# Performance work log

Measured on AMD Instinct MI355X. Metric: run time of the kernel, lower is better.

Reference implementation:

```python
import jax, jax.numpy as jnp
import numpy as np

S = 10  # samples per node


def setup_inputs() -> dict:
    key = jax.random.key(0)
    k1, k2, k3, k4, k5, k6 = jax.random.split(key, 6)
    N, D, V, E, NNZ = 8192, 256, 32768, 100000, 262144
    z = jax.random.normal(k1, (N, D), dtype=jnp.float32)
    W = jax.random.normal(k2, (V, D), dtype=jnp.float32) * 0.02
    rand_u = jax.random.uniform(k3, (N, S), dtype=jnp.float32)
    edges = jax.random.randint(k4, (2, E), 0, N, dtype=jnp.int64)
    ptr = jnp.sort(jax.random.randint(k5, (N + 1,), 0, NNZ, dtype=jnp.int64))
    col = jax.random.randint(k6, (NNZ,), 0, N, dtype=jnp.int64)
    return {"z": z, "W": W, "rand_u": rand_u, "edges": edges, "ptr": ptr, "col": col}


def reference(z, W, rand_u, edges, ptr, col):
    N = z.shape[0]
    nnz = col.shape[0]
    deg = ptr[1:] - ptr[:-1]                                   # [N]
    # vectorized per-node uniform neighbor sampling (with replacement)
    samp = (rand_u * deg[:, None].astype(rand_u.dtype)).astype(jnp.int64)  # [N, S]
    gidx = jnp.clip(ptr[:-1, None] + samp, 0, nnz - 1)          # [N, S]
    self_idx = jnp.arange(N, dtype=col.dtype)[:, None]
    n_u = jnp.where(deg[:, None] > 0, col[gidx], self_idx)      # [N, S]
    # gather-sum aggregation, averaged with self
    u_aggr = (z[n_u].sum(axis=1) + z) / (S + 1)                 # [N, D]
    # predictor: Linear(no bias) + Softmax(dim=1)
    logits = jnp.einsum('nd,vd->nv', u_aggr, W)                 # [N, V]
    probs = jax.nn.softmax(logits, axis=1)
    h_u = probs[edges[0]]                                       # [E, V]
    # nn.CrossEntropyLoss applied to softmax outputs (faithful to original)
    tgt = edges[1]
    log_p = jax.nn.log_softmax(h_u, axis=1)
    loss = -log_p[jnp.arange(tgt.shape[0]), tgt].mean()
    return loss
```

## Files before the change

### kernel.cpp

```cpp
#include <hip/hip_runtime.h>
#include <hip/hip_bf16.h>
#include <stdint.h>


#define NODES 8192
#define DIM   256
#define VOCAB 32768
#define SAMP  10

typedef float  f32x4  __attribute__((ext_vector_type(4)));
typedef short  bf16x8 __attribute__((ext_vector_type(8)));
typedef unsigned short u16x4 __attribute__((ext_vector_type(4)));

static __device__ __forceinline__ unsigned short f2bf(float x) {
    __hip_bfloat16 b = __float2bfloat16(x);
    return *reinterpret_cast<unsigned short*>(&b);
}
static __device__ __forceinline__ float bf2f(unsigned short x) {
    union { unsigned int u; float f; } v; v.u = ((unsigned int)x) << 16; return v.f;
}

__global__ void k_aggregate(const float* __restrict__ z, const float* __restrict__ ru,
                            const int* __restrict__ ptr, const int* __restrict__ col,
                            unsigned short* __restrict__ ub, int nnz) {
    int wid = threadIdx.x >> 6, lane = threadIdx.x & 63;
    int node = blockIdx.x * 4 + wid;
    if (node >= NODES) return;
    int p0 = ptr[node], p1 = ptr[node + 1];
    int deg = p1 - p0;
    float fdeg = (float)deg;
    f32x4 acc = {0.f, 0.f, 0.f, 0.f};
    #pragma unroll
    for (int s = 0; s < SAMP; ++s) {
        float r = ru[node * SAMP + s];
        int samp = (int)(r * fdeg);
        int gidx = p0 + samp;
        gidx = gidx < 0 ? 0 : (gidx > nnz - 1 ? nnz - 1 : gidx);
        int nb = (deg > 0) ? col[gidx] : node;
        acc += ((const f32x4*)(z + (size_t)nb * DIM))[lane];
    }
    acc += ((const f32x4*)(z + (size_t)node * DIM))[lane];
    acc = acc / 11.0f;
    u16x4 h;
    h.x = f2bf(acc.x); h.y = f2bf(acc.y); h.z = f2bf(acc.z); h.w = f2bf(acc.w);
    ((u16x4*)(ub + (size_t)node * DIM))[lane] = h;
}

__global__ void k_convert_w(const float* __restrict__ W, unsigned short* __restrict__ Wb, int n4) {
    int i = blockIdx.x * blockDim.x + threadIdx.x;
    if (i >= n4) return;
    f32x4 v = ((const f32x4*)W)[i];
    u16x4 h;
    h.x = f2bf(v.x); h.y = f2bf(v.y); h.z = f2bf(v.z); h.w = f2bf(v.w);
    ((u16x4*)Wb)[i] = h;
}

#define BM 128
#define BN 256
#define NSTEP 64

static __device__ __forceinline__ void gload_lds16(const void* g, void* l) {
    __builtin_amdgcn_global_load_lds(
        (const __attribute__((address_space(1))) unsigned int*)g,
        (__attribute__((address_space(3))) unsigned int*)l, 16, 0, 0);
}

__global__ __launch_bounds__(512, 2) void k_gemm_stats(
        const unsigned short* __restrict__ A,
        const unsigned short* __restrict__ B,
        float* __restrict__ part_s) {
    __shared__ __align__(16) unsigned short Bs[3][BN * 64];
    __shared__ float sred[BM][4];

    const int bid = blockIdx.x;
    const int slab = bid & 7;
    const int ntile = bid >> 3;
    const int rm = ntile * BM;
    const int cbase = slab * 4096;
    const int t = threadIdx.x;
    const int lane = t & 63;
    const int wid = t >> 6;
    const int wr = wid >> 2, wc = wid & 3;
    const int g = lane >> 4, r16 = lane & 15;

    auto stage = [&](int buf, int step) {
        const int chunk = step >> 2, ks2 = step & 3;
        const int cn = cbase + chunk * BN;
        #pragma unroll
        for (int i = 0; i < 4; ++i) {
            int idx = i * 512 + t;
            int row = idx >> 3;
            int sslot = (idx & 7) ^ (row & 7);
            gload_lds16(B + (size_t)(cn + row) * DIM + ks2 * 64 + sslot * 8,
                        (void*)(&Bs[buf][i * 4096 + t * 8]));
        }
    };

    bf16x8 areg[4][8];
    #pragma unroll
    for (int m = 0; m < 4; ++m)
        #pragma unroll
        for (int j = 0; j < 8; ++j)
            areg[m][j] = *(const bf16x8*)(A +
                (size_t)(rm + wr * 64 + m * 16 + r16) * DIM + (j * 4 + g) * 8);
    stage(0, 0);
    stage(1, 1);

    f32x4 acc[4][4] = {};
    f32x4 sv[4] = {};
    int bcur = 0;

    for (int c = 0; c < 16; ++c) {
        #pragma unroll
        for (int ks = 0; ks < 4; ++ks) {
            const int s = c * 4 + ks;
            asm volatile("s_waitcnt vmcnt(4)" ::: "memory");
            __builtin_amdgcn_s_barrier();
            asm volatile("" ::: "memory");
            if (s + 2 < NSTEP) {
                int bnext = bcur + 2; if (bnext >= 3) bnext -= 3;
                stage(bnext, s + 2);
            }
            __builtin_amdgcn_s_setprio(1);
            #pragma unroll
            for (int kk = 0; kk < 2; ++kk) {
                bf16x8 bfr[4];
                #pragma unroll
                for (int n = 0; n < 4; ++n) {
                    int R = wc * 64 + n * 16 + r16;
                    int slot = (kk * 4 + g) ^ (R & 7);
                    bfr[n] = *(const bf16x8*)(&Bs[bcur][R * 64 + slot * 8]);
                }
                #pragma unroll
                for (int m = 0; m < 4; ++m)
                    #pragma unroll
                    for (int n = 0; n < 4; ++n)
                        acc[m][n] = __builtin_amdgcn_mfma_f32_16x16x32_bf16(
                            areg[m][ks * 2 + kk], bfr[n], acc[m][n], 0, 0, 0);
            }
            __builtin_amdgcn_s_setprio(0);
            bcur = (bcur + 1 == 3) ? 0 : bcur + 1;
            if (ks == 3) {
                #pragma unroll
                for (int m = 0; m < 4; ++m)
                    #pragma unroll
                    for (int n = 0; n < 4; ++n) {
                        #pragma unroll
                        for (int reg = 0; reg < 4; ++reg)
                            sv[m][reg] += __expf(acc[m][n][reg]);
                        acc[m][n] = (f32x4){0.f, 0.f, 0.f, 0.f};
                    }
            }
        }
    }

    #pragma unroll
    for (int m = 0; m < 4; ++m)
        #pragma unroll
        for (int st = 1; st < 16; st <<= 1)
            #pragma unroll
            for (int reg = 0; reg < 4; ++reg)
                sv[m][reg] += __shfl_xor(sv[m][reg], st, 64);
    if (r16 == 0)
        #pragma unroll
        for (int m = 0; m < 4; ++m)
            #pragma unroll
            for (int reg = 0; reg < 4; ++reg)
                sred[wr * 64 + m * 16 + g * 4 + reg][wc] = sv[m][reg];
    __syncthreads();
    if (t < BM)
        part_s[(size_t)(rm + t) * 8 + slab] =
            sred[t][0] + sred[t][1] + sred[t][2] + sred[t][3];
}

__global__ void k_reduce(const float* __restrict__ part_s, float* __restrict__ s0) {
    int n = blockIdx.x * 256 + threadIdx.x;
    float s = 0.f;
    #pragma unroll
    for (int j = 0; j < 8; ++j) s += part_s[(size_t)n * 8 + j];
    s0[n] = s;
}

#define ELB 512
__global__ __launch_bounds__(256) void k_edge_loss(
        const unsigned short* __restrict__ ub, const unsigned short* __restrict__ Wb,
        const int* __restrict__ edges, const float* __restrict__ s0,
        float lse2c, float* __restrict__ partial, int E) {
    int wid = threadIdx.x >> 6, lane = threadIdx.x & 63;
    int w = blockIdx.x * 4 + wid;
    float local = 0.f;
    for (int e = w; e < E; e += ELB * 4) {
        int src = edges[e], tgt = edges[E + e];
        u16x4 a = ((const u16x4*)(ub + (size_t)src * DIM))[lane];
        u16x4 b = ((const u16x4*)(Wb + (size_t)tgt * DIM))[lane];
        float d = bf2f(a.x) * bf2f(b.x) + bf2f(a.y) * bf2f(b.y)
                + bf2f(a.z) * bf2f(b.z) + bf2f(a.w) * bf2f(b.w);
        #pragma unroll
        for (int st = 1; st < 64; st <<= 1) d += __shfl_xor(d, st, 64);
        if (lane == 0) local += lse2c - __expf(d) / s0[src];
    }
    __shared__ float bs[4];
    if (lane == 0) bs[wid] = local;
    __syncthreads();
    if (threadIdx.x == 0) partial[blockIdx.x] = bs[0] + bs[1] + bs[2] + bs[3];
}

__global__ void k_final(const float* __restrict__ partial, float* __restrict__ out, float invE) {
    int t = threadIdx.x;
    float s = partial[t] + partial[t + 256];
    #pragma unroll
    for (int st = 1; st < 64; st <<= 1) s += __shfl_xor(s, st, 64);
    __shared__ float ls[4];
    if ((t & 63) == 0) ls[t >> 6] = s;
    __syncthreads();
    if (t == 0) out[0] = (ls[0] + ls[1] + ls[2] + ls[3]) * invE;
}

extern "C" void kernel_launch(void* const* d_in, const int* in_sizes, int n_in,
                              void* d_out, int out_size, void* d_ws, size_t ws_size,
                              hipStream_t stream) {
    const float* z    = (const float*)d_in[0];
    const float* W    = (const float*)d_in[1];
    const float* ru   = (const float*)d_in[2];
    const int* edges  = (const int*)d_in[3];
    const int* ptr    = (const int*)d_in[4];
    const int* col    = (const int*)d_in[5];
    const int E   = in_sizes[3] / 2;
    const int nnz = in_sizes[5];

    char* ws = (char*)d_ws;
    unsigned short* ub     = (unsigned short*)(ws + 0);
    unsigned short* Wb     = (unsigned short*)(ws + 4194304);
    float*          part_s = (float*)(ws + 20971520);
    float*          s0     = (float*)(ws + 21233664);
    float*          epart  = (float*)(ws + 21266432);
    float*          out    = (float*)d_out;

    const float lse2c = logf((float)VOCAB + 1.0f);

    hipLaunchKernelGGL(k_aggregate, dim3(NODES / 4), dim3(256), 0, stream, z, ru, ptr, col, ub, nnz);
    hipLaunchKernelGGL(k_convert_w, dim3(VOCAB * DIM / 4 / 256), dim3(256), 0, stream, W, Wb, VOCAB * DIM / 4);
    hipLaunchKernelGGL(k_gemm_stats, dim3(512), dim3(512), 0, stream, ub, Wb, part_s);
    hipLaunchKernelGGL(k_reduce, dim3(NODES / 256), dim3(256), 0, stream, part_s, s0);
    hipLaunchKernelGGL(k_edge_loss, dim3(ELB), dim3(256), 0, stream, ub, Wb, edges, s0, lse2c, epart, E);
    hipLaunchKernelGGL(k_final, dim3(1), dim3(256), 0, stream, epart, out, 1.0f / (float)E);
}
```

Baseline: 326.3 us.

## Restructure GEMM B pipeline to double buffer with register prefetch and exp2

Shrinks the LDS B staging from triple to double buffering. Each step now loads B fragments into registers, waits on LDS, barriers, and only then issues the next async global-to-LDS stage, so the buffer can be reused while MFMAs run. The log2(e) factor is folded into the aggregated embedding scale so softmax exponentials use raw v_exp_f32 instead of __expf. Launch bounds are relaxed to one block per SIMD group, and address arithmetic is precomputed as byte offsets. The risks are an extra barrier per step, a possible loss of occupancy, and a slightly different bf16 rounding because of the prescale.

```diff
diff --git a/kernel.cpp b/kernel.cpp
--- a/kernel.cpp
+++ b/kernel.cpp
@@ -7,6 +7,7 @@
 #define DIM   256
 #define VOCAB 32768
 #define SAMP  10
+#define LOG2E 1.4426950408889634f
 
 typedef float  f32x4  __attribute__((ext_vector_type(4)));
 typedef short  bf16x8 __attribute__((ext_vector_type(8)));
@@ -18,6 +19,9 @@
 }
 static __device__ __forceinline__ float bf2f(unsigned short x) {
     union { unsigned int u; float f; } v; v.u = ((unsigned int)x) << 16; return v.f;
+}
+static __device__ __forceinline__ float fexp2(float x) {
+    float r; asm("v_exp_f32 %0, %1" : "=v"(r) : "v"(x)); return r;
 }
 
 __global__ void k_aggregate(const float* __restrict__ z, const float* __restrict__ ru,
@@ -40,7 +44,7 @@
         acc += ((const f32x4*)(z + (size_t)nb * DIM))[lane];
     }
     acc += ((const f32x4*)(z + (size_t)node * DIM))[lane];
-    acc = acc / 11.0f;
+    acc = acc * (LOG2E / 11.0f);
     u16x4 h;
     h.x = f2bf(acc.x); h.y = f2bf(acc.y); h.z = f2bf(acc.z); h.w = f2bf(acc.w);
     ((u16x4*)(ub + (size_t)node * DIM))[lane] = h;
@@ -65,35 +69,35 @@
         (__attribute__((address_space(3))) unsigned int*)l, 16, 0, 0);
 }
 
-__global__ __launch_bounds__(512, 2) void k_gemm_stats(
+__global__ __launch_bounds__(512, 1) void k_gemm_stats(
         const unsigned short* __restrict__ A,
         const unsigned short* __restrict__ B,
         float* __restrict__ part_s) {
-    __shared__ __align__(16) unsigned short Bs[3][BN * 64];
+    __shared__ __align__(16) unsigned short Bs[2][BN * 64];
     __shared__ float sred[BM][4];
 
     const int bid = blockIdx.x;
     const int slab = bid & 7;
     const int ntile = bid >> 3;
     const int rm = ntile * BM;
-    const int cbase = slab * 4096;
     const int t = threadIdx.x;
     const int lane = t & 63;
     const int wid = t >> 6;
     const int wr = wid >> 2, wc = wid & 3;
     const int g = lane >> 4, r16 = lane & 15;
 
-    auto stage = [&](int buf, int step) {
-        const int chunk = step >> 2, ks2 = step & 3;
-        const int cn = cbase + chunk * BN;
-        #pragma unroll
-        for (int i = 0; i < 4; ++i) {
-            int idx = i * 512 + t;
-            int row = idx >> 3;
-            int sslot = (idx & 7) ^ (row & 7);
-            gload_lds16(B + (size_t)(cn + row) * DIM + ks2 * 64 + sslot * 8,
-                        (void*)(&Bs[buf][i * 4096 + t * 8]));
-        }
+    const char* Bbase = (const char*)B + (size_t)slab * (4096u * 512u);
+    const unsigned pre0 = ((unsigned)(t >> 3) << 9)
+                        + ((unsigned)((t & 7) ^ ((t >> 3) & 7)) << 4);
+    const unsigned ldsb = (unsigned)t << 4;
+
+    auto stage = [&](int buf, int sigma) {
+        unsigned soff = ((unsigned)(sigma >> 2) << 17) + ((unsigned)(sigma & 3) << 7);
+        unsigned lb = (unsigned)buf * 32768u + ldsb;
+        #pragma unroll
+        for (int i = 0; i < 4; ++i)
+            gload_lds16(Bbase + soff + pre0 + (unsigned)i * 32768u,
+                        (char*)Bs + lb + (unsigned)i * 8192u);
     };
 
     bf16x8 areg[4][8];
@@ -105,10 +109,22 @@
                 (size_t)(rm + wr * 64 + m * 16 + r16) * DIM + (j * 4 + g) * 8);
     stage(0, 0);
     stage(1, 1);
+    asm volatile("s_waitcnt vmcnt(8)" ::: "memory");
 
     f32x4 acc[4][4] = {};
     f32x4 sv[4] = {};
-    int bcur = 0;
+
+    auto fold = [&]() {
+        #pragma unroll
+        for (int m = 0; m < 4; ++m)
+            #pragma unroll
+            for (int n = 0; n < 4; ++n) {
+                #pragma unroll
+                for (int r = 0; r < 4; ++r)
+                    sv[m][r] += fexp2(acc[m][n][r]);
+                acc[m][n] = (f32x4){0.f, 0.f, 0.f, 0.f};
+            }
+    };
 
     for (int c = 0; c < 16; ++c) {
         #pragma unroll
@@ -116,57 +132,49 @@
             const int s = c * 4 + ks;
             asm volatile("s_waitcnt vmcnt(4)" ::: "memory");
             __builtin_amdgcn_s_barrier();
-            asm volatile("" ::: "memory");
-            if (s + 2 < NSTEP) {
-                int bnext = bcur + 2; if (bnext >= 3) bnext -= 3;
-                stage(bnext, s + 2);
-            }
-            __builtin_amdgcn_s_setprio(1);
-            #pragma unroll
-            for (int kk = 0; kk < 2; ++kk) {
-                bf16x8 bfr[4];
+            const unsigned lbase = (unsigned)(s & 1) * 32768u;
+            bf16x8 bfr[8];
+            #pragma unroll
+            for (int kk = 0; kk < 2; ++kk)
                 #pragma unroll
                 for (int n = 0; n < 4; ++n) {
                     int R = wc * 64 + n * 16 + r16;
                     int slot = (kk * 4 + g) ^ (R & 7);
-                    bfr[n] = *(const bf16x8*)(&Bs[bcur][R * 64 + slot * 8]);
+                    bfr[kk * 4 + n] = *(const bf16x8*)((const char*)Bs
+                        + lbase + (unsigned)(R * 128 + slot * 16));
                 }
+            if (ks == 0 && c > 0) fold();
+            asm volatile("s_waitcnt lgkmcnt(0)" ::: "memory");
+            __builtin_amdgcn_s_barrier();
+            { int sigma = s + 2; if (sigma >= NSTEP) sigma -= NSTEP;
+              stage(s & 1, sigma); }
+            __builtin_amdgcn_s_setprio(1);
+            #pragma unroll
+            for (int kk = 0; kk < 2; ++kk)
                 #pragma unroll
                 for (int m = 0; m < 4; ++m)
                     #pragma unroll
                     for (int n = 0; n < 4; ++n)
                         acc[m][n] = __builtin_amdgcn_mfma_f32_16x16x32_bf16(
-                            areg[m][ks * 2 + kk], bfr[n], acc[m][n], 0, 0, 0);
-            }
+                            areg[m][ks * 2 + kk], bfr[kk * 4 + n], acc[m][n], 0, 0, 0);
             __builtin_amdgcn_s_setprio(0);
-            bcur = (bcur + 1 == 3) ? 0 : bcur + 1;
-            if (ks == 3) {
-                #pragma unroll
-                for (int m = 0; m < 4; ++m)
-                    #pragma unroll
-                    for (int n = 0; n < 4; ++n) {
-                        #pragma unroll
-                        for (int reg = 0; reg < 4; ++reg)
-                            sv[m][reg] += __expf(acc[m][n][reg]);
-                        acc[m][n] = (f32x4){0.f, 0.f, 0.f, 0.f};
-                    }
-            }
         }
     }
+    fold();
 
     #pragma unroll
     for (int m = 0; m < 4; ++m)
         #pragma unroll
         for (int st = 1; st < 16; st <<= 1)
             #pragma unroll
-            for (int reg = 0; reg < 4; ++reg)
-                sv[m][reg] += __shfl_xor(sv[m][reg], st, 64);
+            for (int r = 0; r < 4; ++r)
+                sv[m][r] += __shfl_xor(sv[m][r], st, 64);
     if (r16 == 0)
         #pragma unroll
         for (int m = 0; m < 4; ++m)
             #pragma unroll
-            for (int reg = 0; reg < 4; ++reg)
-                sred[wr * 64 + m * 16 + g * 4 + reg][wc] = sv[m][reg];
+            for (int r = 0; r < 4; ++r)
+                sred[wr * 64 + m * 16 + g * 4 + r][wc] = sv[m][r];
     __syncthreads();
     if (t < BM)
         part_s[(size_t)(rm + t) * 8 + slab] =
@@ -197,7 +205,7 @@
                 + bf2f(a.z) * bf2f(b.z) + bf2f(a.w) * bf2f(b.w);
         #pragma unroll
         for (int st = 1; st < 64; st <<= 1) d += __shfl_xor(d, st, 64);
-        if (lane == 0) local += lse2c - __expf(d) / s0[src];
+        if (lane == 0) local += lse2c - fexp2(d) / s0[src];
     }
     __shared__ float bs[4];
     if (lane == 0) bs[wid] = local;
```

After: 300.6 us. 7.9% less time.
